# Performance work log

Hardware: AMD Instinct MI355X
Metric: run time of the kernel (lower is better)

Reference implementation:

```python
import jax, jax.numpy as jnp
import numpy as np

N, E = 50000, 800000
IN_C, H_C, OUT_C, HEADS = 64, 32, 32, 8


def setup_inputs() -> dict:
    key = jax.random.key(0)
    ks = jax.random.split(key, 16)
    def glorot(k, shape):
        fan_in = shape[-1]
        return jax.random.normal(k, shape, dtype=jnp.float32) / jnp.sqrt(jnp.float32(fan_in))
    inp = {
        'x': jax.random.normal(ks[0], (N, IN_C), dtype=jnp.float32),
        'edge_index': jax.random.randint(ks[1], (2, E), 0, N, dtype=jnp.int64),
        # layer 1: in_c -> h_c, heads
        'W1l': glorot(ks[2], (HEADS * H_C, IN_C)),
        'b1l': jnp.zeros((HEADS * H_C,), jnp.float32),
        'W1r': glorot(ks[3], (HEADS * H_C, IN_C)),
        'b1r': jnp.zeros((HEADS * H_C,), jnp.float32),
        'att1': glorot(ks[4], (HEADS, H_C)),
        'bias1': jnp.zeros((H_C,), jnp.float32),
        # layer 2: h_c -> out_c, heads
        'W2l': glorot(ks[5], (HEADS * OUT_C, H_C)),
        'b2l': jnp.zeros((HEADS * OUT_C,), jnp.float32),
        'W2r': glorot(ks[6], (HEADS * OUT_C, H_C)),
        'b2r': jnp.zeros((HEADS * OUT_C,), jnp.float32),
        'att2': glorot(ks[7], (HEADS, OUT_C)),
        'bias2': jnp.zeros((OUT_C,), jnp.float32),
    }
    return inp


def _gatv2_layer(x, src, dst, valid, Wl, bl, Wr, br, att, bias):
    # PyG GATv2Conv (share_weights=False, concat=False): message j->i uses
    # e = att . leaky_relu(lin_l(x_j) + lin_r(x_i), 0.2); softmax over dst; agg lin_l(x_j).
    n = x.shape[0]
    heads, c = att.shape
    xl = (x @ Wl.T + bl).reshape(n, heads, c)
    xr = (x @ Wr.T + br).reshape(n, heads, c)
    m = jax.nn.leaky_relu(xl[src] + xr[dst], negative_slope=0.2)  # [Etot,H,C]
    score = jnp.einsum('ehc,hc->eh', m, att)                      # [Etot,H]
    score = jnp.where(valid[:, None], score, -jnp.inf)
    smax = jax.ops.segment_max(score, dst, num_segments=n)        # [N,H]
    a = jnp.where(valid[:, None], jnp.exp(score - smax[dst]), 0.0)
    denom = jax.ops.segment_sum(a, dst, num_segments=n)
    a = a / jnp.maximum(denom[dst], 1e-16)
    out = jax.ops.segment_sum(a[..., None] * xl[src], dst, num_segments=n)  # [N,H,C]
    return out.mean(axis=1) + bias


def reference(x, edge_index, W1l, b1l, W1r, b1r, att1, bias1,
              W2l, b2l, W2r, b2r, att2, bias2):
    n = x.shape[0]
    src0, dst0 = edge_index[0], edge_index[1]
    # PyG removes existing self loops then adds fresh ones: mask originals,
    # append one self loop per node (keeps static shapes).
    loop = jnp.arange(n, dtype=src0.dtype)
    src = jnp.concatenate([src0, loop])
    dst = jnp.concatenate([dst0, loop])
    valid = jnp.concatenate([src0 != dst0, jnp.ones((n,), bool)])
    h = _gatv2_layer(x, src, dst, valid, W1l, b1l, W1r, b1r, att1, bias1)
    h = jax.nn.leaky_relu(h, negative_slope=0.01)  # nn.LeakyReLU default
    out = _gatv2_layer(h, src, dst, valid, W2l, b2l, W2r, b2r, att2, bias2)
    return out
```

## Files before the change

kernel.cpp:

```cpp
#include <hip/hip_runtime.h>
#include <math.h>

#define HEADS 8
#define CDIM 32
#define ODIM 256
#define BKT_SHIFT 7
#define CHUNK 2048

typedef _Float16 h2 __attribute__((ext_vector_type(2)));
typedef _Float16 h4 __attribute__((ext_vector_type(4)));
typedef _Float16 h8 __attribute__((ext_vector_type(8)));
typedef float f32x4 __attribute__((ext_vector_type(4)));
union H4 { h4 v; h2 p[2]; };

#if __has_builtin(__builtin_amdgcn_fdot2)
#define FDOT2(a,b,c) __builtin_amdgcn_fdot2((a),(b),(c),false)
#else
static __device__ __forceinline__ float fdot2_sw(h2 a, h2 b, float c){
  return fmaf((float)a.x, (float)b.x, fmaf((float)a.y, (float)b.y, c));
}
#define FDOT2(a,b,c) fdot2_sw((a),(b),(c))
#endif

__device__ __forceinline__ float lrelu(float v, float s){ return fmaxf(v, s*v); }


__global__ __launch_bounds__(256) void csr_hist_kernel(
    const int* __restrict__ src, const int* __restrict__ dst,
    int* __restrict__ rank, int* __restrict__ hist, int e, int B){
  __shared__ int lh[512];
  int t = threadIdx.x, k = blockIdx.x;
  for (int b = t; b < B; b += 256) lh[b] = 0;
  __syncthreads();
  int base_i = k*CHUNK;
#pragma unroll
  for (int j = 0; j < CHUNK/256; ++j){
    int i = base_i + j*256 + t;
    if (i < e){
      int s = src[i], d = dst[i];
      int r = -1;
      if (s != d) r = atomicAdd(&lh[d>>BKT_SHIFT], 1);
      rank[i] = r;
    }
  }
  __syncthreads();
  for (int b = t; b < B; b += 256) hist[k*B + b] = lh[b];
}

__global__ __launch_bounds__(512) void csr_offs_kernel(
    int* __restrict__ hist, int* __restrict__ btotal, int NB, int B){
  __shared__ int s[512];
  int b = blockIdx.x, t = threadIdx.x;
  int v = (t < NB) ? hist[t*B + b] : 0;
  s[t] = v;
  __syncthreads();
  for (int off=1; off<512; off<<=1){
    int u = (t >= off) ? s[t-off] : 0;
    __syncthreads(); s[t] += u; __syncthreads();
  }
  int excl = s[t] - v;
  if (t < NB) hist[t*B + b] = excl;
  if (t == NB-1) btotal[b] = excl + v;
}

__global__ __launch_bounds__(512) void csr_base_kernel(
    const int* __restrict__ btotal, int* __restrict__ base, int B){
  __shared__ int s[512];
  int t = threadIdx.x;
  int v = (t < B) ? btotal[t] : 0;
  s[t] = v;
  __syncthreads();
  for (int off=1; off<512; off<<=1){
    int u = (t >= off) ? s[t-off] : 0;
    __syncthreads(); s[t] += u; __syncthreads();
  }
  if (t < B) base[t] = s[t] - v;
  if (t == B-1) base[B] = s[t];
}

__global__ __launch_bounds__(256) void csr_scatter_kernel(
    const int* __restrict__ src, const int* __restrict__ dst,
    const int* __restrict__ rank, const int* __restrict__ offs,
    const int* __restrict__ base, int* __restrict__ bpack, int e, int B){
  int t = threadIdx.x, k = blockIdx.x;
  int base_i = k*CHUNK;
#pragma unroll
  for (int j = 0; j < CHUNK/256; ++j){
    int i = base_i + j*256 + t;
    if (i < e){
      int r = rank[i];
      if (r >= 0){
        int d = dst[i], s = src[i];
        int b = d >> BKT_SHIFT;
        int pos = base[b] + offs[k*B + b] + r;
        bpack[pos] = (s << BKT_SHIFT) | (d & 127);
      }
    }
  }
}

__global__ __launch_bounds__(256) void csr_sort_kernel(
    const int* __restrict__ bpack, const int* __restrict__ base,
    int* __restrict__ csr, int* __restrict__ indptr, int n, int B){
  __shared__ int lh[128], cur[128], ss[128];
  int b = blockIdx.x, t = threadIdx.x;
  int beg = base[b], cnt = base[b+1] - beg;
  if (t < 128) lh[t] = 0;
  __syncthreads();
  for (int j = t; j < cnt; j += 256){
    int p = bpack[beg + j];
    atomicAdd(&lh[p & 127], 1);
  }
  __syncthreads();
  int v = (t < 128) ? lh[t] : 0;
  if (t < 128) ss[t] = v;
  __syncthreads();
  for (int off=1; off<128; off<<=1){
    int u = (t >= off && t < 128) ? ss[t-off] : 0;
    __syncthreads();
    if (t < 128) ss[t] += u;
    __syncthreads();
  }
  if (t < 128){
    int excl = ss[t] - v;
    cur[t] = excl;
    int node = (b << BKT_SHIFT) + t;
    if (node <= n) indptr[node] = beg + excl;
  }
  __syncthreads();
  for (int j = t; j < cnt; j += 256){
    int p = bpack[beg + j];
    int lpos = atomicAdd(&cur[p & 127], 1);
    csr[beg + lpos] = p >> BKT_SHIFT;
  }
}

template<int K, bool FUSE_COUNT>
__global__ __launch_bounds__(256, 2) void gemm_mfma(const float* __restrict__ X,
    const float* __restrict__ Wl, const float* __restrict__ bl,
    const float* __restrict__ Wr, const float* __restrict__ br,
    _Float16* __restrict__ outl, _Float16* __restrict__ outr, int n){
  const int KP = K + 8;
  __shared__ __align__(16) _Float16 Xs[64*(K+8)];
  int t = threadIdx.x;
  int n0 = blockIdx.x*64;
  int ybase = blockIdx.y;

  for (int idx = t; idx < 64*(K/4); idx += 256){
    int row = idx/(K/4), c = (idx%(K/4))*4;
    int node = n0 + row; if (node >= n) node = n-1;
    float4 xv = *(const float4*)(X + (size_t)node*K + c);
    h4 hv = {(_Float16)xv.x, (_Float16)xv.y, (_Float16)xv.z, (_Float16)xv.w};
    *(h4*)(Xs + row*KP + c) = hv;
  }
  __syncthreads();

  int wave = t >> 6, lane = t & 63;
  int co = ybase*256 + wave*64;
  const float* W   = (co < 256) ? Wl : Wr;
  const float* Bv  = (co < 256) ? bl : br;
  _Float16* outp   = (co < 256) ? outl : outr;
  int lco = co & 255;
  int lr = lane & 15, lg = lane >> 4;

  f32x4 acc[4][4];
#pragma unroll
  for (int c = 0; c < 4; ++c)
#pragma unroll
    for (int m = 0; m < 4; ++m) acc[c][m] = (f32x4){0.f, 0.f, 0.f, 0.f};

#pragma unroll
  for (int ks = 0; ks < K/32; ++ks){
    int k0 = ks*32 + lg*8;
    h8 a[4], b[4];
#pragma unroll
    for (int c = 0; c < 4; ++c){
      const float* wp = W + (size_t)(lco + c*16 + lr)*K + k0;
      float4 w0 = *(const float4*)(wp);
      float4 w1 = *(const float4*)(wp + 4);
      a[c] = (h8){(_Float16)w0.x,(_Float16)w0.y,(_Float16)w0.z,(_Float16)w0.w,
                  (_Float16)w1.x,(_Float16)w1.y,(_Float16)w1.z,(_Float16)w1.w};
    }
#pragma unroll
    for (int m = 0; m < 4; ++m)
      b[m] = *(const h8*)(Xs + (m*16 + lr)*KP + k0);
#pragma unroll
    for (int c = 0; c < 4; ++c)
#pragma unroll
      for (int m = 0; m < 4; ++m)
        acc[c][m] = __builtin_amdgcn_mfma_f32_16x16x32_f16(a[c], b[m], acc[c][m], 0, 0, 0);
  }

#pragma unroll
  for (int c = 0; c < 4; ++c){
    int ch = lco + c*16 + lg*4;
    float4 bb = *(const float4*)(Bv + ch);
#pragma unroll
    for (int m = 0; m < 4; ++m){
      int node = n0 + m*16 + lr;
      if (node < n){
        h4 o = {(_Float16)(acc[c][m][0] + bb.x), (_Float16)(acc[c][m][1] + bb.y),
                (_Float16)(acc[c][m][2] + bb.z), (_Float16)(acc[c][m][3] + bb.w)};
        *(h4*)(outp + (size_t)node*ODIM + ch) = o;
      }
    }
  }
}

__global__ __launch_bounds__(256) void edge_kernel(
    const _Float16* __restrict__ xl, const _Float16* __restrict__ xr,
    const float* __restrict__ att, const float* __restrict__ bias,
    const int* __restrict__ indptr, const int* __restrict__ csr_src,
    float* __restrict__ out, int n, int act)
{
  int wid = blockIdx.x*4 + (threadIdx.x >> 6);
  if (wid >= n) return;
  int lane = threadIdx.x & 63;
  const float LOG2E = 1.44269504088896341f;

  float4 attf = *(const float4*)(att + 4*lane);
  h2 at0 = (h2){(_Float16)(attf.x*LOG2E), (_Float16)(attf.y*LOG2E)};
  h2 at1 = (h2){(_Float16)(attf.z*LOG2E), (_Float16)(attf.w*LOG2E)};
  const h2 c02 = {(_Float16)0.2f, (_Float16)0.2f};

  H4 xrh; xrh.v = *(const h4*)(xr + (size_t)wid*ODIM + 4*lane);
  H4 self; self.v = *(const h4*)(xl + (size_t)wid*ODIM + 4*lane);

  auto score = [&](const H4& c)->float{
    h2 t0 = c.p[0] + xrh.p[0];
    h2 t1 = c.p[1] + xrh.p[1];
    h2 q0 = __builtin_elementwise_max(t0, t0 * c02);
    h2 q1 = __builtin_elementwise_max(t1, t1 * c02);
    float d = FDOT2(q0, at0, FDOT2(q1, at1, 0.f));
    d += __shfl_xor(d, 1);
    d += __shfl_xor(d, 2);
    d += __shfl_xor(d, 4);
    return d;
  };

  float w0 = exp2f(score(self));
  float denom = w0;
  float4 acc;
  acc.x = w0 * (float)self.v.x;
  acc.y = w0 * (float)self.v.y;
  acc.z = w0 * (float)self.v.z;
  acc.w = w0 * (float)self.v.w;

  int beg = __builtin_amdgcn_readfirstlane(indptr[wid]);
  int end = __builtin_amdgcn_readfirstlane(indptr[wid+1]);
  int cnt = end - beg;
  H4 r0, r1;
  r0.v = (h4){}; r1.v = (h4){};
  if (cnt > 0){
    int s0 = __builtin_amdgcn_readfirstlane(csr_src[beg]);
    r0.v = *(const h4*)(xl + (size_t)s0*ODIM + 4*lane);
  }
  if (cnt > 1){
    int s1 = __builtin_amdgcn_readfirstlane(csr_src[beg+1]);
    r1.v = *(const h4*)(xl + (size_t)s1*ODIM + 4*lane);
  }
  for (int k = 0; k < cnt; ++k){
    H4 cur = r0; r0 = r1;
    if (k+2 < cnt){
      int s2 = __builtin_amdgcn_readfirstlane(csr_src[beg+k+2]);
      r1.v = *(const h4*)(xl + (size_t)s2*ODIM + 4*lane);
    }
    float pe = exp2f(score(cur));
    denom += pe;
    acc.x = fmaf(pe, (float)cur.v.x, acc.x);
    acc.y = fmaf(pe, (float)cur.v.y, acc.y);
    acc.z = fmaf(pe, (float)cur.v.z, acc.z);
    acc.w = fmaf(pe, (float)cur.v.w, acc.w);
  }
  float inv = 1.f/denom;
  float vx = acc.x*inv, vy = acc.y*inv, vz = acc.z*inv, vw = acc.w*inv;
  vx += __shfl_xor(vx, 8);  vx += __shfl_xor(vx, 16);  vx += __shfl_xor(vx, 32);
  vy += __shfl_xor(vy, 8);  vy += __shfl_xor(vy, 16);  vy += __shfl_xor(vy, 32);
  vz += __shfl_xor(vz, 8);  vz += __shfl_xor(vz, 16);  vz += __shfl_xor(vz, 32);
  vw += __shfl_xor(vw, 8);  vw += __shfl_xor(vw, 16);  vw += __shfl_xor(vw, 32);
  if (lane < 8){
    float4 bv = *(const float4*)(bias + 4*lane);
    float ox = vx*0.125f + bv.x;
    float oy = vy*0.125f + bv.y;
    float oz = vz*0.125f + bv.z;
    float ow = vw*0.125f + bv.w;
    if (act){
      ox = lrelu(ox, 0.01f); oy = lrelu(oy, 0.01f);
      oz = lrelu(oz, 0.01f); ow = lrelu(ow, 0.01f);
    }
    *(float4*)(out + (size_t)wid*CDIM + 4*lane) = make_float4(ox, oy, oz, ow);
  }
}

extern "C" void kernel_launch(void* const* d_in, const int* in_sizes, int n_in,
                              void* d_out, int out_size, void* d_ws, size_t ws_size,
                              hipStream_t stream){
  (void)n_in; (void)out_size; (void)ws_size;
  const float* x    = (const float*)d_in[0];
  const int*   ei   = (const int*)d_in[1];
  const float* W1l  = (const float*)d_in[2];
  const float* b1l  = (const float*)d_in[3];
  const float* W1r  = (const float*)d_in[4];
  const float* b1r  = (const float*)d_in[5];
  const float* att1 = (const float*)d_in[6];
  const float* bias1= (const float*)d_in[7];
  const float* W2l  = (const float*)d_in[8];
  const float* b2l  = (const float*)d_in[9];
  const float* W2r  = (const float*)d_in[10];
  const float* b2r  = (const float*)d_in[11];
  const float* att2 = (const float*)d_in[12];
  const float* bias2= (const float*)d_in[13];
  int n = in_sizes[0] / 64;
  int e = in_sizes[1] / 2;
  const int* src = ei;
  const int* dst = ei + e;

  char* ws = (char*)d_ws;
  size_t off = 0;
  auto alloc = [&](size_t bytes)->char*{
    char* p = ws + off; off += (bytes + 255) & ~(size_t)255; return p;
  };
  _Float16* xl  = (_Float16*)alloc((size_t)n*ODIM*2);
  _Float16* xr  = (_Float16*)alloc((size_t)n*ODIM*2);
  float* h      = (float*)alloc((size_t)n*CDIM*4);
  int*   indptr = (int*)alloc((size_t)(n+1)*4);
  int*   rank   = (int*)alloc((size_t)e*4);
  int*   csr    = (int*)alloc((size_t)e*4);
  int*   bpack  = (int*)alloc((size_t)e*4);

  int NB = (e + CHUNK-1) / CHUNK;
  int B  = (n + 127) >> 7;
  int*   hist   = (int*)alloc((size_t)NB*B*4);
  int*   btotal = (int*)alloc((size_t)B*4);
  int*   base   = (int*)alloc((size_t)(B+1)*4);

  int nt64 = (n + 63) / 64;

  csr_hist_kernel<<<NB, 256, 0, stream>>>(src, dst, rank, hist, e, B);
  csr_offs_kernel<<<B, 512, 0, stream>>>(hist, btotal, NB, B);
  csr_base_kernel<<<1, 512, 0, stream>>>(btotal, base, B);
  csr_scatter_kernel<<<NB, 256, 0, stream>>>(src, dst, rank, hist, base, bpack, e, B);
  csr_sort_kernel<<<B, 256, 0, stream>>>(bpack, base, csr, indptr, n, B);

  gemm_mfma<64,false><<<dim3(nt64,2), 256, 0, stream>>>(
      x, W1l, b1l, W1r, b1r, xl, xr, n);
  edge_kernel<<<(n+3)/4, 256, 0, stream>>>(xl, xr, att1, bias1, indptr, csr, h, n, 1);
  gemm_mfma<32,false><<<dim3(nt64,2), 256, 0, stream>>>(
      h, W2l, b2l, W2r, b2r, xl, xr, n);
  edge_kernel<<<(n+3)/4, 256, 0, stream>>>(xl, xr, att2, bias2, indptr, csr, (float*)d_out, n, 0);
}
```

Baseline: 320.0 us.

## Fuse CSR histogram into layer-1 GEMM launch and batch edge index loads

Result: faster. 310.5 us (-2.9%).

```diff
diff --git a/kernel.cpp b/kernel.cpp
--- a/kernel.cpp
+++ b/kernel.cpp
@@ -24,28 +24,6 @@
 
 __device__ __forceinline__ float lrelu(float v, float s){ return fmaxf(v, s*v); }
 
-
-__global__ __launch_bounds__(256) void csr_hist_kernel(
-    const int* __restrict__ src, const int* __restrict__ dst,
-    int* __restrict__ rank, int* __restrict__ hist, int e, int B){
-  __shared__ int lh[512];
-  int t = threadIdx.x, k = blockIdx.x;
-  for (int b = t; b < B; b += 256) lh[b] = 0;
-  __syncthreads();
-  int base_i = k*CHUNK;
-#pragma unroll
-  for (int j = 0; j < CHUNK/256; ++j){
-    int i = base_i + j*256 + t;
-    if (i < e){
-      int s = src[i], d = dst[i];
-      int r = -1;
-      if (s != d) r = atomicAdd(&lh[d>>BKT_SHIFT], 1);
-      rank[i] = r;
-    }
-  }
-  __syncthreads();
-  for (int b = t; b < B; b += 256) hist[k*B + b] = lh[b];
-}
 
 __global__ __launch_bounds__(512) void csr_offs_kernel(
     int* __restrict__ hist, int* __restrict__ btotal, int NB, int B){
@@ -135,11 +113,36 @@
   }
 }
 
-template<int K, bool FUSE_COUNT>
+template<int K, bool FUSE_HIST>
 __global__ __launch_bounds__(256, 2) void gemm_mfma(const float* __restrict__ X,
     const float* __restrict__ Wl, const float* __restrict__ bl,
     const float* __restrict__ Wr, const float* __restrict__ br,
-    _Float16* __restrict__ outl, _Float16* __restrict__ outr, int n){
+    _Float16* __restrict__ outl, _Float16* __restrict__ outr, int n,
+    const int* __restrict__ src, const int* __restrict__ dst,
+    int* __restrict__ rank, int* __restrict__ hist, int e, int B){
+  if (FUSE_HIST && blockIdx.y == 2){
+    int k = blockIdx.x;
+    int NB = (e + CHUNK-1)/CHUNK;
+    if (k >= NB) return;
+    __shared__ int lh[512];
+    int t = threadIdx.x;
+    for (int b = t; b < B; b += 256) lh[b] = 0;
+    __syncthreads();
+    int base_i = k*CHUNK;
+#pragma unroll
+    for (int j = 0; j < CHUNK/256; ++j){
+      int i = base_i + j*256 + t;
+      if (i < e){
+        int s = src[i], d = dst[i];
+        int r = -1;
+        if (s != d) r = atomicAdd(&lh[d>>BKT_SHIFT], 1);
+        rank[i] = r;
+      }
+    }
+    __syncthreads();
+    for (int b = t; b < B; b += 256) hist[k*B + b] = lh[b];
+    return;
+  }
   const int KP = K + 8;
   __shared__ __align__(16) _Float16 Xs[64*(K+8)];
   int t = threadIdx.x;
@@ -249,29 +252,36 @@
   int beg = __builtin_amdgcn_readfirstlane(indptr[wid]);
   int end = __builtin_amdgcn_readfirstlane(indptr[wid+1]);
   int cnt = end - beg;
-  H4 r0, r1;
-  r0.v = (h4){}; r1.v = (h4){};
-  if (cnt > 0){
-    int s0 = __builtin_amdgcn_readfirstlane(csr_src[beg]);
-    r0.v = *(const h4*)(xl + (size_t)s0*ODIM + 4*lane);
-  }
-  if (cnt > 1){
-    int s1 = __builtin_amdgcn_readfirstlane(csr_src[beg+1]);
-    r1.v = *(const h4*)(xl + (size_t)s1*ODIM + 4*lane);
-  }
-  for (int k = 0; k < cnt; ++k){
-    H4 cur = r0; r0 = r1;
-    if (k+2 < cnt){
-      int s2 = __builtin_amdgcn_readfirstlane(csr_src[beg+k+2]);
-      r1.v = *(const h4*)(xl + (size_t)s2*ODIM + 4*lane);
-    }
-    float pe = exp2f(score(cur));
-    denom += pe;
-    acc.x = fmaf(pe, (float)cur.v.x, acc.x);
-    acc.y = fmaf(pe, (float)cur.v.y, acc.y);
-    acc.z = fmaf(pe, (float)cur.v.z, acc.z);
-    acc.w = fmaf(pe, (float)cur.v.w, acc.w);
-  }
+
+#define GATHER(j) (*(const h4*)(xl + (size_t)((unsigned)__shfl(sidx,(j)))*ODIM + 4*lane))
+  for (int cb = 0; cb < cnt; cb += 64){
+    int ccnt = min(cnt - cb, 64);
+    int sidx = (lane < ccnt) ? csr_src[beg + cb + lane] : 0;
+    H4 r0, r1, r2, r3;
+    r0.v = (h4){}; r1.v = (h4){}; r2.v = (h4){}; r3.v = (h4){};
+    if (ccnt > 0) r0.v = GATHER(0);
+    if (ccnt > 1) r1.v = GATHER(1);
+    if (ccnt > 2) r2.v = GATHER(2);
+    if (ccnt > 3) r3.v = GATHER(3);
+#pragma unroll 2
+    for (int k = 0; k < ccnt; k += 2){
+      H4 e0 = r0, e1 = r1;
+      r0 = r2; r1 = r3;
+      if (k+4 < ccnt) r2.v = GATHER(k+4);
+      if (k+5 < ccnt) r3.v = GATHER(k+5);
+      float s0 = score(e0);
+      float s1 = score(e1);
+      float pe0 = exp2f(s0);
+      float pe1 = (k+1 < ccnt) ? exp2f(s1) : 0.f;
+      denom += pe0 + pe1;
+      acc.x = fmaf(pe0, (float)e0.v.x, fmaf(pe1, (float)e1.v.x, acc.x));
+      acc.y = fmaf(pe0, (float)e0.v.y, fmaf(pe1, (float)e1.v.y, acc.y));
+      acc.z = fmaf(pe0, (float)e0.v.z, fmaf(pe1, (float)e1.v.z, acc.z));
+      acc.w = fmaf(pe0, (float)e0.v.w, fmaf(pe1, (float)e1.v.w, acc.w));
+    }
+  }
+#undef GATHER
+
   float inv = 1.f/denom;
   float vx = acc.x*inv, vy = acc.y*inv, vz = acc.z*inv, vw = acc.w*inv;
   vx += __shfl_xor(vx, 8);  vx += __shfl_xor(vx, 16);  vx += __shfl_xor(vx, 32);
@@ -336,16 +346,15 @@
 
   int nt64 = (n + 63) / 64;
 
-  csr_hist_kernel<<<NB, 256, 0, stream>>>(src, dst, rank, hist, e, B);
+  gemm_mfma<64,true><<<dim3(nt64,3), 256, 0, stream>>>(
+      x, W1l, b1l, W1r, b1r, xl, xr, n, src, dst, rank, hist, e, B);
   csr_offs_kernel<<<B, 512, 0, stream>>>(hist, btotal, NB, B);
   csr_base_kernel<<<1, 512, 0, stream>>>(btotal, base, B);
   csr_scatter_kernel<<<NB, 256, 0, stream>>>(src, dst, rank, hist, base, bpack, e, B);
   csr_sort_kernel<<<B, 256, 0, stream>>>(bpack, base, csr, indptr, n, B);
 
-  gemm_mfma<64,false><<<dim3(nt64,2), 256, 0, stream>>>(
-      x, W1l, b1l, W1r, b1r, xl, xr, n);
   edge_kernel<<<(n+3)/4, 256, 0, stream>>>(xl, xr, att1, bias1, indptr, csr, h, n, 1);
   gemm_mfma<32,false><<<dim3(nt64,2), 256, 0, stream>>>(
-      h, W2l, b2l, W2r, b2r, xl, xr, n);
+      h, W2l, b2l, W2r, b2r, xl, xr, n, nullptr, nullptr, nullptr, nullptr, 0, 0);
   edge_kernel<<<(n+3)/4, 256, 0, stream>>>(xl, xr, att2, bias2, indptr, csr, (float*)d_out, n, 0);
 }
```
